# Kernel optimization log

Hardware: AMD Instinct MI355X
Metric: run time of the kernel (lower is better)

The kernel has to match this reference:

```python
import jax, jax.numpy as jnp
import numpy as np

N = 8192          # number of nodes
IN_F = 256        # in_features
OUT_F = 128       # out_features
ALPHA = 0.2       # LeakyReLU negative slope


def setup_inputs() -> dict:
    key = jax.random.key(0)
    k1, k2, k3, k4 = jax.random.split(key, 4)
    h = jax.random.normal(k1, (N, IN_F), dtype=jnp.float32)
    adj = jax.random.randint(k2, (N, N), 0, 2, dtype=jnp.int32)  # dense 0/1 adjacency mask
    W = (jax.random.normal(k3, (IN_F, OUT_F), dtype=jnp.float32) * 0.05)   # W.weight^T
    a = (jax.random.normal(k4, (2 * OUT_F,), dtype=jnp.float32) * 0.05)    # a.weight flattened
    return {"h": h, "adj": adj, "W": W, "a": a}


def reference(h, adj, W, a):
    # Wh = self.W(h): [N, OUT_F]
    Wh = h @ W
    # Original builds an [N, N, 2F] concat tensor then projects with 'a'.
    # Equivalent math: e[i, j] = leaky_relu(Wh[i]@a1 + Wh[j]@a2)
    a1, a2 = a[:OUT_F], a[OUT_F:]
    src = Wh @ a1                                     # [N] per-source score
    dst = Wh @ a2                                     # [N] per-target score
    e = jax.nn.leaky_relu(src[:, None] + dst[None, :], negative_slope=ALPHA)  # [N, N]
    # masked softmax over neighbors (dim=1); adj==0 -> -inf
    e = jnp.where(adj == 0, -jnp.inf, e)
    attention = jax.nn.softmax(e, axis=1)             # [N, N]
    # dropout p=0 in eval-mode reference -> identity
    h_prime = attention @ Wh                          # [N, OUT_F]
    return jax.nn.elu(h_prime)                        # concat=True -> ELU
```

## Files before the change

### kernel.cpp

```cpp
#include <hip/hip_runtime.h>
#include <math.h>

#define N 8192
#define IN_F 256
#define OUT_F 128
#define ALPHA 0.2f

typedef _Float16 f16;
typedef __attribute__((ext_vector_type(4))) float f32x4;
typedef __attribute__((ext_vector_type(8))) _Float16 f16x8;
typedef __attribute__((ext_vector_type(4))) _Float16 f16x4;

__global__ __launch_bounds__(256) void k_prep(const float* __restrict__ W,
                                              f16* __restrict__ WT) {
    int idx = blockIdx.x * 256 + threadIdx.x;
    int f = idx >> 8;
    int k = idx & 255;
    WT[idx] = (f16)W[k * OUT_F + f];
}

#define HS 280
__global__ __launch_bounds__(256) void k_wh(const float* __restrict__ h,
                                            const f16* __restrict__ WT,
                                            const float* __restrict__ a,
                                            f16* __restrict__ WhT,
                                            float* __restrict__ src,
                                            float* __restrict__ dst) {
    __shared__ __align__(16) f16 hA[32][HS];
    __shared__ __align__(16) f16 outT[128][40];
    __shared__ float sred[4][32], dred[4][32];

    const int t = threadIdx.x;
    const int i0 = blockIdx.x * 32;
    const int wv = t >> 6, l = t & 63, ln = l & 15, lq = l >> 4;

    {
        const float4* hg = (const float4*)(h + (size_t)i0 * IN_F);
#pragma unroll
        for (int it = 0; it < 8; ++it) {
            int idx = t + it * 256;
            int r = idx >> 6;
            int c4 = (idx & 63) * 4;
            float4 v = hg[idx];
            f16x4 p = { (f16)v.x, (f16)v.y, (f16)v.z, (f16)v.w };
            *(f16x4*)&hA[r][c4] = p;
        }
    }
    __syncthreads();

    f32x4 acc00 = {0.f,0.f,0.f,0.f}, acc01 = {0.f,0.f,0.f,0.f};
    f32x4 acc10 = {0.f,0.f,0.f,0.f}, acc11 = {0.f,0.f,0.f,0.f};
    const int f0 = 32 * wv;

#pragma unroll
    for (int ks = 0; ks < 8; ++ks) {
        const int k0 = 32 * ks + 8 * lq;
        f16x8 a0 = *(const f16x8*)&hA[ln][k0];
        f16x8 a1 = *(const f16x8*)&hA[16 + ln][k0];
        f16x8 b0 = *(const f16x8*)(WT + (size_t)(f0 + ln) * IN_F + k0);
        f16x8 b1 = *(const f16x8*)(WT + (size_t)(f0 + 16 + ln) * IN_F + k0);
        acc00 = __builtin_amdgcn_mfma_f32_16x16x32_f16(a0, b0, acc00, 0, 0, 0);
        acc01 = __builtin_amdgcn_mfma_f32_16x16x32_f16(a0, b1, acc01, 0, 0, 0);
        acc10 = __builtin_amdgcn_mfma_f32_16x16x32_f16(a1, b0, acc10, 0, 0, 0);
        acc11 = __builtin_amdgcn_mfma_f32_16x16x32_f16(a1, b1, acc11, 0, 0, 0);
    }

    const float a1c0 = a[f0 + ln],      a2c0 = a[128 + f0 + ln];
    const float a1c1 = a[f0 + 16 + ln], a2c1 = a[128 + f0 + 16 + ln];
    float sp[8], dp[8];
#pragma unroll
    for (int i = 0; i < 8; ++i) { sp[i] = 0.f; dp[i] = 0.f; }

#pragma unroll
    for (int hh = 0; hh < 2; ++hh) {
        f32x4 v0 = hh ? acc10 : acc00;
        f32x4 v1 = hh ? acc11 : acc01;
        f16x4 p0, p1;
#pragma unroll
        for (int rg = 0; rg < 4; ++rg) {
            sp[hh * 4 + rg] += v0[rg] * a1c0 + v1[rg] * a1c1;
            dp[hh * 4 + rg] += v0[rg] * a2c0 + v1[rg] * a2c1;
            p0[rg] = (f16)v0[rg];
            p1[rg] = (f16)v1[rg];
        }
        *(f16x4*)&outT[f0 + ln][16 * hh + 4 * lq] = p0;
        *(f16x4*)&outT[f0 + 16 + ln][16 * hh + 4 * lq] = p1;
    }
#pragma unroll
    for (int i = 0; i < 8; ++i) {
        float s = sp[i], d = dp[i];
        s += __shfl_down(s, 8, 16); d += __shfl_down(d, 8, 16);
        s += __shfl_down(s, 4, 16); d += __shfl_down(d, 4, 16);
        s += __shfl_down(s, 2, 16); d += __shfl_down(d, 2, 16);
        s += __shfl_down(s, 1, 16); d += __shfl_down(d, 1, 16);
        if (ln == 0) {
            int row = 16 * (i >> 2) + 4 * lq + (i & 3);
            sred[wv][row] = s;
            dred[wv][row] = d;
        }
    }
    __syncthreads();
    if (t < 32) {
        src[i0 + t] = sred[0][t] + sred[1][t] + sred[2][t] + sred[3][t];
        dst[i0 + t] = dred[0][t] + dred[1][t] + dred[2][t] + dred[3][t];
    }
    {
        const int col = t & 127, g = t >> 7;
        f16x8 q0 = *(const f16x8*)&outT[col][16 * g];
        f16x8 q1 = *(const f16x8*)&outT[col][16 * g + 8];
        *(f16x8*)(WhT + (size_t)col * N + i0 + 16 * g) = q0;
        *(f16x8*)(WhT + (size_t)col * N + i0 + 16 * g + 8) = q1;
    }
}

#define TI 32
#define NJ 128
#define NC (N / NJ)
#define WSTRIDE 152
__global__ __launch_bounds__(512) void k_attn(const int* __restrict__ adj,
                                              const f16* __restrict__ WhT,
                                              const float* __restrict__ src,
                                              const float* __restrict__ dst,
                                              float* __restrict__ out) {
    __shared__ __align__(16) f16 wA[2][TI][WSTRIDE];
    __shared__ float lfin[TI];

    const int t = threadIdx.x;
    const int i0 = blockIdx.x * TI;
    const int pr = t >> 4;
    const int pm = t & 15;
    const int wv = t >> 6;
    const int l = t & 63, ln = l & 15, lq = l >> 4;

    const float my_src = src[i0 + pr];
    const float cshift = fabsf(my_src) + 4.0f;
    float lp = 0.f;
    f32x4 accv0 = {0.f,0.f,0.f,0.f}, accv1 = {0.f,0.f,0.f,0.f};

    const int* arow = adj + (size_t)(i0 + pr) * N;
    const f16* Bb = WhT + (size_t)(16 * wv + ln) * N + 8 * lq;

    int4 aA0, aB0, aA1, aB1;
    float4 dA0, dB0, dA1, dB1;

    auto issue = [&](int c, int4& xA, int4& xB, float4& xdA, float4& xdB) {
        const int j0 = c * NJ + 8 * pm;
        xA = *(const int4*)(arow + j0);
        xB = *(const int4*)(arow + j0 + 4);
        xdA = *(const float4*)(dst + j0);
        xdB = *(const float4*)(dst + j0 + 4);
    };
    auto produce = [&](int c, const int4& xA, const int4& xB,
                       const float4& xdA, const float4& xdB) {
        float w[8];
        const int*   av = (const int*)&xA;
        const int*   bv = (const int*)&xB;
        const float* df = (const float*)&xdA;
        const float* ef = (const float*)&xdB;
#pragma unroll
        for (int k = 0; k < 4; ++k) {
            float e = my_src + df[k];
            float lk = e > 0.f ? e : ALPHA * e;
            w[k] = av[k] ? __expf(lk - cshift) : 0.f;
        }
#pragma unroll
        for (int k = 0; k < 4; ++k) {
            float e = my_src + ef[k];
            float lk = e > 0.f ? e : ALPHA * e;
            w[4 + k] = bv[k] ? __expf(lk - cshift) : 0.f;
        }
        f16x8 wp;
#pragma unroll
        for (int k = 0; k < 8; ++k) { lp += w[k]; wp[k] = (f16)w[k]; }
        *(f16x8*)&wA[c & 1][pr][8 * pm] = wp;
    };
    auto mpass = [&](int c) {
        const f16* wb = &wA[c & 1][0][0];
        const f16* bp = Bb + c * NJ;
#pragma unroll
        for (int ks = 0; ks < 4; ++ks) {
            const int k0 = 32 * ks;
            f16x8 bf = *(const f16x8*)(bp + k0);
            f16x8 a0 = *(const f16x8*)(wb + ln * WSTRIDE + k0 + 8 * lq);
            f16x8 a1 = *(const f16x8*)(wb + (16 + ln) * WSTRIDE + k0 + 8 * lq);
            accv0 = __builtin_amdgcn_mfma_f32_16x16x32_f16(a0, bf, accv0, 0, 0, 0);
            accv1 = __builtin_amdgcn_mfma_f32_16x16x32_f16(a1, bf, accv1, 0, 0, 0);
        }
    };

    issue(0, aA0, aB0, dA0, dB0);
    produce(0, aA0, aB0, dA0, dB0);
    issue(1, aA1, aB1, dA1, dB1);
    __syncthreads();

    for (int cc = 0; cc < NC; cc += 2) {
        if (cc + 2 < NC) issue(cc + 2, aA0, aB0, dA0, dB0);
        mpass(cc);
        produce(cc + 1, aA1, aB1, dA1, dB1);
        __syncthreads();
        if (cc + 3 < NC) issue(cc + 3, aA1, aB1, dA1, dB1);
        mpass(cc + 1);
        if (cc + 2 < NC) produce(cc + 2, aA0, aB0, dA0, dB0);
        __syncthreads();
    }

    {
        float v = lp;
        v += __shfl_down(v, 8, 16);
        v += __shfl_down(v, 4, 16);
        v += __shfl_down(v, 2, 16);
        v += __shfl_down(v, 1, 16);
        if (pm == 0) lfin[pr] = v;
    }
    __syncthreads();

#pragma unroll
    for (int hh = 0; hh < 2; ++hh) {
        f32x4 av = hh ? accv1 : accv0;
#pragma unroll
        for (int rg = 0; rg < 4; ++rg) {
            const int row = 16 * hh + 4 * lq + rg;
            float hp = av[rg] / lfin[row];
            float res = hp > 0.f ? hp : expm1f(hp);
            out[(size_t)(i0 + row) * OUT_F + 16 * wv + ln] = res;
        }
    }
}

extern "C" void kernel_launch(void* const* d_in, const int* in_sizes, int n_in,
                              void* d_out, int out_size, void* d_ws, size_t ws_size,
                              hipStream_t stream) {
    const float* h   = (const float*)d_in[0];
    const int*   adj = (const int*)d_in[1];
    const float* W   = (const float*)d_in[2];
    const float* a   = (const float*)d_in[3];
    float* out = (float*)d_out;

    f16*   WT  = (f16*)d_ws;
    f16*   WhT = (f16*)((char*)d_ws + (1 << 16));
    float* src = (float*)((char*)WhT + (size_t)OUT_F * N * sizeof(f16));
    float* dst = src + N;

    k_prep<<<128, 256, 0, stream>>>(W, WT);
    k_wh<<<N / 32, 256, 0, stream>>>(h, WT, a, WhT, src, dst);
    k_attn<<<N / TI, 512, 0, stream>>>(adj, WhT, src, dst, out);
}
```

Before: 418.7 us.

## Split attention over column segments with register-only MFMA tiles and combine pass

Rewrites the attention kernel so that each wave computes its softmax weights directly in registers in MFMA A-operand layout, with no LDS staging and no block barriers. Each wave covers 32 rows and all 128 output features, so every WhT fragment it loads is reused across 16 MFMAs. The j dimension is split into 8 segments to give 512 blocks; partial outputs and row sums go to workspace and a new combine kernel applies normalisation and ELU. Adjacency is read with nontemporal loads and LeakyReLU is computed branch-free. The cost is extra workspace traffic for the partials (about 32MB), one more kernel launch, and high register pressure from 64 accumulator registers per thread.

```diff
diff --git a/kernel.cpp b/kernel.cpp
--- a/kernel.cpp
+++ b/kernel.cpp
@@ -6,10 +6,15 @@
 #define OUT_F 128
 #define ALPHA 0.2f
 
+#define SEG 8
+#define JSEG (N / SEG)
+#define CHN (JSEG / 32)
+
 typedef _Float16 f16;
 typedef __attribute__((ext_vector_type(4))) float f32x4;
 typedef __attribute__((ext_vector_type(8))) _Float16 f16x8;
 typedef __attribute__((ext_vector_type(4))) _Float16 f16x4;
+typedef __attribute__((ext_vector_type(4))) int i32x4;
 
 __global__ __launch_bounds__(256) void k_prep(const float* __restrict__ W,
                                               f16* __restrict__ WT) {
@@ -113,118 +118,144 @@
     }
 }
 
-#define TI 32
-#define NJ 128
-#define NC (N / NJ)
-#define WSTRIDE 152
-__global__ __launch_bounds__(512) void k_attn(const int* __restrict__ adj,
+__global__ __launch_bounds__(256) void k_attn(const int* __restrict__ adj,
                                               const f16* __restrict__ WhT,
                                               const float* __restrict__ src,
                                               const float* __restrict__ dst,
+                                              float* __restrict__ part,
+                                              float* __restrict__ lpPart) {
+    const int t = threadIdx.x;
+    const int wv = t >> 6, l = t & 63, ln = l & 15, lq = l >> 4;
+    const int bid = blockIdx.x;
+    const int s  = bid & (SEG - 1);
+    const int rg = bid >> 3;
+    const int R0 = rg * 128 + wv * 32;
+    const int jb = s * JSEG;
+
+    const float src0 = src[R0 + ln],      src1 = src[R0 + 16 + ln];
+    const float csh0 = fabsf(src0) + 4.0f, csh1 = fabsf(src1) + 4.0f;
+
+    const int*   __restrict__ ar0 = adj + (size_t)(R0 + ln) * N + jb + 8 * lq;
+    const int*   __restrict__ ar1 = adj + (size_t)(R0 + 16 + ln) * N + jb + 8 * lq;
+    const float* __restrict__ dp  = dst + jb + 8 * lq;
+    const f16*   __restrict__ Bp  = WhT + (size_t)ln * N + jb + 8 * lq;
+
+    f32x4 acc0[8], acc1[8];
+#pragma unroll
+    for (int i = 0; i < 8; ++i) {
+        acc0[i] = (f32x4){0.f, 0.f, 0.f, 0.f};
+        acc1[i] = (f32x4){0.f, 0.f, 0.f, 0.f};
+    }
+    float lp0 = 0.f, lp1 = 0.f;
+
+    i32x4 aA00, aA01, aA10, aA11, aB00, aB01, aB10, aB11;
+    f32x4 dA0, dA1, dB0, dB1;
+
+#define ISSUE(c, A00, A01, A10, A11, D0, D1)                                   \
+    {                                                                          \
+        const int o = (c) * 32;                                                \
+        A00 = __builtin_nontemporal_load((const i32x4*)(ar0 + o));             \
+        A01 = __builtin_nontemporal_load((const i32x4*)(ar0 + o + 4));         \
+        A10 = __builtin_nontemporal_load((const i32x4*)(ar1 + o));             \
+        A11 = __builtin_nontemporal_load((const i32x4*)(ar1 + o + 4));         \
+        D0  = *(const f32x4*)(dp + o);                                         \
+        D1  = *(const f32x4*)(dp + o + 4);                                     \
+    }
+
+    auto cw = [&](const i32x4& A00, const i32x4& A01, const i32x4& A10, const i32x4& A11,
+                  const f32x4& D0, const f32x4& D1, f16x8& w0, f16x8& w1) {
+#pragma unroll
+        for (int k = 0; k < 4; ++k) {
+            float e, lk, v;
+            e = src0 + D0[k]; lk = fmaf(0.4f, fabsf(e), 0.6f * e);
+            v = A00[k] ? __expf(lk - csh0) : 0.f; lp0 += v; w0[k] = (f16)v;
+            e = src0 + D1[k]; lk = fmaf(0.4f, fabsf(e), 0.6f * e);
+            v = A01[k] ? __expf(lk - csh0) : 0.f; lp0 += v; w0[4 + k] = (f16)v;
+            e = src1 + D0[k]; lk = fmaf(0.4f, fabsf(e), 0.6f * e);
+            v = A10[k] ? __expf(lk - csh1) : 0.f; lp1 += v; w1[k] = (f16)v;
+            e = src1 + D1[k]; lk = fmaf(0.4f, fabsf(e), 0.6f * e);
+            v = A11[k] ? __expf(lk - csh1) : 0.f; lp1 += v; w1[4 + k] = (f16)v;
+        }
+    };
+
+    ISSUE(0, aA00, aA01, aA10, aA11, dA0, dA1);
+    ISSUE(1, aB00, aB01, aB10, aB11, dB0, dB1);
+
+    for (int c = 0; c < CHN; c += 2) {
+        {
+            const f16* bp = Bp + c * 32;
+            f16x8 b[8];
+#pragma unroll
+            for (int ft = 0; ft < 8; ++ft)
+                b[ft] = *(const f16x8*)(bp + (size_t)(16 * ft) * N);
+            f16x8 w0, w1;
+            cw(aA00, aA01, aA10, aA11, dA0, dA1, w0, w1);
+            if (c + 2 < CHN) ISSUE(c + 2, aA00, aA01, aA10, aA11, dA0, dA1);
+#pragma unroll
+            for (int ft = 0; ft < 8; ++ft) {
+                acc0[ft] = __builtin_amdgcn_mfma_f32_16x16x32_f16(w0, b[ft], acc0[ft], 0, 0, 0);
+                acc1[ft] = __builtin_amdgcn_mfma_f32_16x16x32_f16(w1, b[ft], acc1[ft], 0, 0, 0);
+            }
+        }
+        {
+            const f16* bp = Bp + (c + 1) * 32;
+            f16x8 b[8];
+#pragma unroll
+            for (int ft = 0; ft < 8; ++ft)
+                b[ft] = *(const f16x8*)(bp + (size_t)(16 * ft) * N);
+            f16x8 w0, w1;
+            cw(aB00, aB01, aB10, aB11, dB0, dB1, w0, w1);
+            if (c + 3 < CHN) ISSUE(c + 3, aB00, aB01, aB10, aB11, dB0, dB1);
+#pragma unroll
+            for (int ft = 0; ft < 8; ++ft) {
+                acc0[ft] = __builtin_amdgcn_mfma_f32_16x16x32_f16(w0, b[ft], acc0[ft], 0, 0, 0);
+                acc1[ft] = __builtin_amdgcn_mfma_f32_16x16x32_f16(w1, b[ft], acc1[ft], 0, 0, 0);
+            }
+        }
+    }
+#undef ISSUE
+
+    lp0 += __shfl_xor(lp0, 16); lp0 += __shfl_xor(lp0, 32);
+    lp1 += __shfl_xor(lp1, 16); lp1 += __shfl_xor(lp1, 32);
+    if (l < 16) {
+        lpPart[(size_t)s * N + R0 + ln]      = lp0;
+        lpPart[(size_t)s * N + R0 + 16 + ln] = lp1;
+    }
+
+    float* __restrict__ pp = part + ((size_t)s * N + R0) * OUT_F;
+#pragma unroll
+    for (int ft = 0; ft < 8; ++ft)
+#pragma unroll
+        for (int r = 0; r < 4; ++r) {
+            pp[(size_t)(4 * lq + r) * OUT_F + 16 * ft + ln]        = acc0[ft][r];
+            pp[(size_t)(16 + 4 * lq + r) * OUT_F + 16 * ft + ln]   = acc1[ft][r];
+        }
+}
+
+__global__ __launch_bounds__(256) void k_comb(const float* __restrict__ part,
+                                              const float* __restrict__ lpPart,
                                               float* __restrict__ out) {
-    __shared__ __align__(16) f16 wA[2][TI][WSTRIDE];
-    __shared__ float lfin[TI];
-
-    const int t = threadIdx.x;
-    const int i0 = blockIdx.x * TI;
-    const int pr = t >> 4;
-    const int pm = t & 15;
-    const int wv = t >> 6;
-    const int l = t & 63, ln = l & 15, lq = l >> 4;
-
-    const float my_src = src[i0 + pr];
-    const float cshift = fabsf(my_src) + 4.0f;
-    float lp = 0.f;
-    f32x4 accv0 = {0.f,0.f,0.f,0.f}, accv1 = {0.f,0.f,0.f,0.f};
-
-    const int* arow = adj + (size_t)(i0 + pr) * N;
-    const f16* Bb = WhT + (size_t)(16 * wv + ln) * N + 8 * lq;
-
-    int4 aA0, aB0, aA1, aB1;
-    float4 dA0, dB0, dA1, dB1;
-
-    auto issue = [&](int c, int4& xA, int4& xB, float4& xdA, float4& xdB) {
-        const int j0 = c * NJ + 8 * pm;
-        xA = *(const int4*)(arow + j0);
-        xB = *(const int4*)(arow + j0 + 4);
-        xdA = *(const float4*)(dst + j0);
-        xdB = *(const float4*)(dst + j0 + 4);
-    };
-    auto produce = [&](int c, const int4& xA, const int4& xB,
-                       const float4& xdA, const float4& xdB) {
-        float w[8];
-        const int*   av = (const int*)&xA;
-        const int*   bv = (const int*)&xB;
-        const float* df = (const float*)&xdA;
-        const float* ef = (const float*)&xdB;
-#pragma unroll
-        for (int k = 0; k < 4; ++k) {
-            float e = my_src + df[k];
-            float lk = e > 0.f ? e : ALPHA * e;
-            w[k] = av[k] ? __expf(lk - cshift) : 0.f;
-        }
-#pragma unroll
-        for (int k = 0; k < 4; ++k) {
-            float e = my_src + ef[k];
-            float lk = e > 0.f ? e : ALPHA * e;
-            w[4 + k] = bv[k] ? __expf(lk - cshift) : 0.f;
-        }
-        f16x8 wp;
-#pragma unroll
-        for (int k = 0; k < 8; ++k) { lp += w[k]; wp[k] = (f16)w[k]; }
-        *(f16x8*)&wA[c & 1][pr][8 * pm] = wp;
-    };
-    auto mpass = [&](int c) {
-        const f16* wb = &wA[c & 1][0][0];
-        const f16* bp = Bb + c * NJ;
-#pragma unroll
-        for (int ks = 0; ks < 4; ++ks) {
-            const int k0 = 32 * ks;
-            f16x8 bf = *(const f16x8*)(bp + k0);
-            f16x8 a0 = *(const f16x8*)(wb + ln * WSTRIDE + k0 + 8 * lq);
-            f16x8 a1 = *(const f16x8*)(wb + (16 + ln) * WSTRIDE + k0 + 8 * lq);
-            accv0 = __builtin_amdgcn_mfma_f32_16x16x32_f16(a0, bf, accv0, 0, 0, 0);
-            accv1 = __builtin_amdgcn_mfma_f32_16x16x32_f16(a1, bf, accv1, 0, 0, 0);
-        }
-    };
-
-    issue(0, aA0, aB0, dA0, dB0);
-    produce(0, aA0, aB0, dA0, dB0);
-    issue(1, aA1, aB1, dA1, dB1);
-    __syncthreads();
-
-    for (int cc = 0; cc < NC; cc += 2) {
-        if (cc + 2 < NC) issue(cc + 2, aA0, aB0, dA0, dB0);
-        mpass(cc);
-        produce(cc + 1, aA1, aB1, dA1, dB1);
-        __syncthreads();
-        if (cc + 3 < NC) issue(cc + 3, aA1, aB1, dA1, dB1);
-        mpass(cc + 1);
-        if (cc + 2 < NC) produce(cc + 2, aA0, aB0, dA0, dB0);
-        __syncthreads();
-    }
-
-    {
-        float v = lp;
-        v += __shfl_down(v, 8, 16);
-        v += __shfl_down(v, 4, 16);
-        v += __shfl_down(v, 2, 16);
-        v += __shfl_down(v, 1, 16);
-        if (pm == 0) lfin[pr] = v;
-    }
-    __syncthreads();
-
-#pragma unroll
-    for (int hh = 0; hh < 2; ++hh) {
-        f32x4 av = hh ? accv1 : accv0;
-#pragma unroll
-        for (int rg = 0; rg < 4; ++rg) {
-            const int row = 16 * hh + 4 * lq + rg;
-            float hp = av[rg] / lfin[row];
-            float res = hp > 0.f ? hp : expm1f(hp);
-            out[(size_t)(i0 + row) * OUT_F + 16 * wv + ln] = res;
-        }
-    }
+    const int idx = blockIdx.x * 256 + threadIdx.x;
+    const int row = idx >> 5;
+    const int c4  = idx & 31;
+
+    float lsum = 0.f;
+#pragma unroll
+    for (int s = 0; s < SEG; ++s) lsum += lpPart[(size_t)s * N + row];
+
+    f32x4 v = {0.f, 0.f, 0.f, 0.f};
+#pragma unroll
+    for (int s = 0; s < SEG; ++s)
+        v += *(const f32x4*)(part + ((size_t)s * N + row) * OUT_F + c4 * 4);
+
+    const float inv = 1.0f / lsum;
+    f32x4 r;
+#pragma unroll
+    for (int k = 0; k < 4; ++k) {
+        float hp = v[k] * inv;
+        r[k] = hp > 0.f ? hp : expm1f(hp);
+    }
+    *(f32x4*)(out + (size_t)row * OUT_F + c4 * 4) = r;
 }
 
 extern "C" void kernel_launch(void* const* d_in, const int* in_sizes, int n_in,
@@ -240,8 +271,11 @@
     f16*   WhT = (f16*)((char*)d_ws + (1 << 16));
     float* src = (float*)((char*)WhT + (size_t)OUT_F * N * sizeof(f16));
     float* dst = src + N;
+    float* lpP = dst + N;
+    float* part = (float*)((char*)d_ws + (8u << 20));
 
     k_prep<<<128, 256, 0, stream>>>(W, WT);
     k_wh<<<N / 32, 256, 0, stream>>>(h, WT, a, WhT, src, dst);
-    k_attn<<<N / TI, 512, 0, stream>>>(adj, WhT, src, dst, out);
-}
+    k_attn<<<(N / 128) * SEG, 256, 0, stream>>>(adj, WhT, src, dst, part, lpP);
+    k_comb<<<(N * OUT_F / 4) / 256, 256, 0, stream>>>(part, lpP, out);
+}
```

Result: no change. 424.1 us (+1.3%).

## Restructure attention kernel to 16-row tiles with 512-wide chunks and swizzled LDS

Applied to the files above, without the earlier changes.

The attention kernel now gives each block 16 rows instead of 32, with each wave producing two rows over 512-column chunks. The 16 per-chunk iterations replace 64 smaller ones, cutting the number of barriers. Shared memory writes use an XOR swizzle to avoid bank conflicts, and LeakyReLU is computed branch-free with fabs/fma. The trade-off is that WhT is reread from L2 twice as often (once per 16 rows rather than 32), and the launch bounds request higher occupancy.

```diff
diff --git a/kernel.cpp b/kernel.cpp
--- a/kernel.cpp
+++ b/kernel.cpp
@@ -6,10 +6,14 @@
 #define OUT_F 128
 #define ALPHA 0.2f
 
+#define NJC 512
+#define NCH (N / NJC)
+
 typedef _Float16 f16;
 typedef __attribute__((ext_vector_type(4))) float f32x4;
 typedef __attribute__((ext_vector_type(8))) _Float16 f16x8;
 typedef __attribute__((ext_vector_type(4))) _Float16 f16x4;
+typedef __attribute__((ext_vector_type(4))) int i32x4;
 
 __global__ __launch_bounds__(256) void k_prep(const float* __restrict__ W,
                                               f16* __restrict__ WT) {
@@ -113,117 +117,107 @@
     }
 }
 
-#define TI 32
-#define NJ 128
-#define NC (N / NJ)
-#define WSTRIDE 152
-__global__ __launch_bounds__(512) void k_attn(const int* __restrict__ adj,
-                                              const f16* __restrict__ WhT,
-                                              const float* __restrict__ src,
-                                              const float* __restrict__ dst,
-                                              float* __restrict__ out) {
-    __shared__ __align__(16) f16 wA[2][TI][WSTRIDE];
-    __shared__ float lfin[TI];
+__global__ __launch_bounds__(512, 4) void k_attn(const int* __restrict__ adj,
+                                                 const f16* __restrict__ WhT,
+                                                 const float* __restrict__ src,
+                                                 const float* __restrict__ dst,
+                                                 float* __restrict__ out) {
+    __shared__ __align__(16) f16 wA[2][16][NJC];
+    __shared__ float lfin[16];
 
     const int t = threadIdx.x;
-    const int i0 = blockIdx.x * TI;
-    const int pr = t >> 4;
-    const int pm = t & 15;
-    const int wv = t >> 6;
-    const int l = t & 63, ln = l & 15, lq = l >> 4;
-
-    const float my_src = src[i0 + pr];
-    const float cshift = fabsf(my_src) + 4.0f;
-    float lp = 0.f;
-    f32x4 accv0 = {0.f,0.f,0.f,0.f}, accv1 = {0.f,0.f,0.f,0.f};
-
-    const int* arow = adj + (size_t)(i0 + pr) * N;
-    const f16* Bb = WhT + (size_t)(16 * wv + ln) * N + 8 * lq;
-
-    int4 aA0, aB0, aA1, aB1;
-    float4 dA0, dB0, dA1, dB1;
-
-    auto issue = [&](int c, int4& xA, int4& xB, float4& xdA, float4& xdB) {
-        const int j0 = c * NJ + 8 * pm;
-        xA = *(const int4*)(arow + j0);
-        xB = *(const int4*)(arow + j0 + 4);
-        xdA = *(const float4*)(dst + j0);
-        xdB = *(const float4*)(dst + j0 + 4);
+    const int wv = t >> 6, l = t & 63, ln = l & 15, lq = l >> 4;
+    const int R0 = blockIdx.x * 16;
+    const int r0 = 2 * wv, r1 = 2 * wv + 1;
+
+    const float s0 = src[R0 + r0],     s1 = src[R0 + r1];
+    const float c0 = fabsf(s0) + 4.f,  c1 = fabsf(s1) + 4.f;
+
+    const int*   __restrict__ a0p = adj + (size_t)(R0 + r0) * N + 4 * l;
+    const int*   __restrict__ a1p = adj + (size_t)(R0 + r1) * N + 4 * l;
+    const float* __restrict__ dpp = dst + 4 * l;
+    const f16*   __restrict__ Bp  = WhT + (size_t)(16 * wv + ln) * N + 8 * lq;
+
+    f32x4 acc = {0.f, 0.f, 0.f, 0.f};
+    float lp0 = 0.f, lp1 = 0.f;
+
+    i32x4 A0a, A0b, A1a, A1b;
+    f32x4 D0, D1;
+
+    char* const wbase = (char*)&wA[0][0][0];
+    auto waddr = [&](int buf, int r, int byteInRow) -> char* {
+        return wbase + buf * (16 * NJC * 2) + (((r * (NJC * 2)) + byteInRow) ^ ((r & 7) << 4));
     };
-    auto produce = [&](int c, const int4& xA, const int4& xB,
-                       const float4& xdA, const float4& xdB) {
-        float w[8];
-        const int*   av = (const int*)&xA;
-        const int*   bv = (const int*)&xB;
-        const float* df = (const float*)&xdA;
-        const float* ef = (const float*)&xdB;
+
+#define ISSUE(c)                                                               \
+    {                                                                          \
+        const int o = (c) * NJC;                                               \
+        A0a = *(const i32x4*)(a0p + o);                                        \
+        A0b = *(const i32x4*)(a0p + o + 256);                                  \
+        A1a = *(const i32x4*)(a1p + o);                                        \
+        A1b = *(const i32x4*)(a1p + o + 256);                                  \
+        D0  = *(const f32x4*)(dpp + o);                                        \
+        D1  = *(const f32x4*)(dpp + o + 256);                                  \
+    }
+
+    auto produce = [&](int c) {
+        const int buf = c & 1;
+        f16x4 w0a, w0b, w1a, w1b;
 #pragma unroll
         for (int k = 0; k < 4; ++k) {
-            float e = my_src + df[k];
-            float lk = e > 0.f ? e : ALPHA * e;
-            w[k] = av[k] ? __expf(lk - cshift) : 0.f;
-        }
-#pragma unroll
-        for (int k = 0; k < 4; ++k) {
-            float e = my_src + ef[k];
-            float lk = e > 0.f ? e : ALPHA * e;
-            w[4 + k] = bv[k] ? __expf(lk - cshift) : 0.f;
-        }
-        f16x8 wp;
-#pragma unroll
-        for (int k = 0; k < 8; ++k) { lp += w[k]; wp[k] = (f16)w[k]; }
-        *(f16x8*)&wA[c & 1][pr][8 * pm] = wp;
+            float e, lk, v;
+            e = s0 + D0[k]; lk = fmaf(0.4f, fabsf(e), 0.6f * e);
+            v = A0a[k] ? __expf(lk - c0) : 0.f; lp0 += v; w0a[k] = (f16)v;
+            e = s0 + D1[k]; lk = fmaf(0.4f, fabsf(e), 0.6f * e);
+            v = A0b[k] ? __expf(lk - c0) : 0.f; lp0 += v; w0b[k] = (f16)v;
+            e = s1 + D0[k]; lk = fmaf(0.4f, fabsf(e), 0.6f * e);
+            v = A1a[k] ? __expf(lk - c1) : 0.f; lp1 += v; w1a[k] = (f16)v;
+            e = s1 + D1[k]; lk = fmaf(0.4f, fabsf(e), 0.6f * e);
+            v = A1b[k] ? __expf(lk - c1) : 0.f; lp1 += v; w1b[k] = (f16)v;
+        }
+        *(f16x4*)waddr(buf, r0, 8 * l)       = w0a;
+        *(f16x4*)waddr(buf, r0, 8 * l + 512) = w0b;
+        *(f16x4*)waddr(buf, r1, 8 * l)       = w1a;
+        *(f16x4*)waddr(buf, r1, 8 * l + 512) = w1b;
     };
+
     auto mpass = [&](int c) {
-        const f16* wb = &wA[c & 1][0][0];
-        const f16* bp = Bb + c * NJ;
-#pragma unroll
-        for (int ks = 0; ks < 4; ++ks) {
-            const int k0 = 32 * ks;
-            f16x8 bf = *(const f16x8*)(bp + k0);
-            f16x8 a0 = *(const f16x8*)(wb + ln * WSTRIDE + k0 + 8 * lq);
-            f16x8 a1 = *(const f16x8*)(wb + (16 + ln) * WSTRIDE + k0 + 8 * lq);
-            accv0 = __builtin_amdgcn_mfma_f32_16x16x32_f16(a0, bf, accv0, 0, 0, 0);
-            accv1 = __builtin_amdgcn_mfma_f32_16x16x32_f16(a1, bf, accv1, 0, 0, 0);
+        const int buf = c & 1;
+        const f16* bp = Bp + c * NJC;
+#pragma unroll
+        for (int ks = 0; ks < NJC / 32; ++ks) {
+            f16x8 b = *(const f16x8*)(bp + 32 * ks);
+            f16x8 a = *(const f16x8*)waddr(buf, ln, 64 * ks + 16 * lq);
+            acc = __builtin_amdgcn_mfma_f32_16x16x32_f16(a, b, acc, 0, 0, 0);
         }
     };
 
-    issue(0, aA0, aB0, dA0, dB0);
-    produce(0, aA0, aB0, dA0, dB0);
-    issue(1, aA1, aB1, dA1, dB1);
-    __syncthreads();
-
-    for (int cc = 0; cc < NC; cc += 2) {
-        if (cc + 2 < NC) issue(cc + 2, aA0, aB0, dA0, dB0);
-        mpass(cc);
-        produce(cc + 1, aA1, aB1, dA1, dB1);
+    ISSUE(0);
+    produce(0);
+    __syncthreads();
+
+    for (int c = 0; c < NCH; ++c) {
+        if (c + 1 < NCH) ISSUE(c + 1);
+        mpass(c);
+        if (c + 1 < NCH) produce(c + 1);
         __syncthreads();
-        if (cc + 3 < NC) issue(cc + 3, aA1, aB1, dA1, dB1);
-        mpass(cc + 1);
-        if (cc + 2 < NC) produce(cc + 2, aA0, aB0, dA0, dB0);
-        __syncthreads();
-    }
-
-    {
-        float v = lp;
-        v += __shfl_down(v, 8, 16);
-        v += __shfl_down(v, 4, 16);
-        v += __shfl_down(v, 2, 16);
-        v += __shfl_down(v, 1, 16);
-        if (pm == 0) lfin[pr] = v;
-    }
-    __syncthreads();
-
-#pragma unroll
-    for (int hh = 0; hh < 2; ++hh) {
-        f32x4 av = hh ? accv1 : accv0;
-#pragma unroll
-        for (int rg = 0; rg < 4; ++rg) {
-            const int row = 16 * hh + 4 * lq + rg;
-            float hp = av[rg] / lfin[row];
-            float res = hp > 0.f ? hp : expm1f(hp);
-            out[(size_t)(i0 + row) * OUT_F + 16 * wv + ln] = res;
-        }
+    }
+#undef ISSUE
+
+#pragma unroll
+    for (int off = 32; off; off >>= 1) {
+        lp0 += __shfl_xor(lp0, off);
+        lp1 += __shfl_xor(lp1, off);
+    }
+    if (l == 0) { lfin[r0] = lp0; lfin[r1] = lp1; }
+    __syncthreads();
+
+#pragma unroll
+    for (int r = 0; r < 4; ++r) {
+        const int row = 4 * lq + r;
+        float hp = acc[r] / lfin[row];
+        float res = hp > 0.f ? hp : expm1f(hp);
+        out[(size_t)(R0 + row) * OUT_F + 16 * wv + ln] = res;
     }
 }
 
@@ -243,5 +237,5 @@
 
     k_prep<<<128, 256, 0, stream>>>(W, WT);
     k_wh<<<N / 32, 256, 0, stream>>>(h, WT, a, WhT, src, dst);
-    k_attn<<<N / TI, 512, 0, stream>>>(adj, WhT, src, dst, out);
-}
+    k_attn<<<N / 16, 512, 0, stream>>>(adj, WhT, src, dst, out);
+}
```

After: 448.2 us. 1.07x slower.
